# Optimization experiments

Hardware: AMD Instinct MI355X
Metric: run time of the kernel (lower is better)

The kernel has to match this reference:

```python
import jax, jax.numpy as jnp
import numpy as np

B, NQ, C = 2, 10000, 256
M, L, K = 8, 3, 4
D = C // M
LEVEL_SHAPES = [(100, 100), (50, 50), (25, 25)]


def setup_inputs() -> dict:
    key = jax.random.key(0)
    ks = jax.random.split(key, 16)
    inp = {
        "query": jax.random.normal(ks[0], (B, NQ, C), jnp.float32),
        "reference_points": jax.random.uniform(ks[1], (B, NQ, 2), jnp.float32),
        "value0": jax.random.normal(ks[2], (B, C) + LEVEL_SHAPES[0], jnp.float32),
        "value1": jax.random.normal(ks[3], (B, C) + LEVEL_SHAPES[1], jnp.float32),
        "value2": jax.random.normal(ks[4], (B, C) + LEVEL_SHAPES[2], jnp.float32),
        "Wv": jax.random.normal(ks[5], (C, C), jnp.float32) * 0.02,
        "bv": jnp.zeros((C,), jnp.float32),
        "Ws": jax.random.normal(ks[6], (M * L * K * 2, C), jnp.float32) * 0.05,
        "bs": jax.random.normal(ks[7], (M * L * K * 2,), jnp.float32),
        "Wa": jax.random.normal(ks[8], (M * L * K, C), jnp.float32) * 0.02,
        "ba": jnp.zeros((M * L * K,), jnp.float32),
        "Wo": jax.random.normal(ks[9], (C, C), jnp.float32) * 0.02,
        "bo": jnp.zeros((C,), jnp.float32),
    }
    return inp


def _bilinear_sample(vflat, px, py, H, W):
    """grid_sample bilinear, align_corners=False, padding_mode='zeros'.
    vflat: (B, M, H*W, D); px, py: (B, M, Q, K) pixel coords. -> (B, M, Q, K, D)
    """
    b, m, q, k = px.shape
    x0 = jnp.floor(px)
    y0 = jnp.floor(py)
    wx1 = px - x0  # frac weights (grad 1 w.r.t. px, matching grid_sample)
    wy1 = py - y0
    wx0 = 1.0 - wx1
    wy0 = 1.0 - wy1

    def gather(xi, yi):
        valid = ((xi >= 0) & (xi <= W - 1) & (yi >= 0) & (yi <= H - 1)).astype(vflat.dtype)
        xc = jnp.clip(xi, 0, W - 1).astype(jnp.int32)
        yc = jnp.clip(yi, 0, H - 1).astype(jnp.int32)
        idx = (yc * W + xc).reshape(b, m, q * k)
        g = jnp.take_along_axis(vflat, idx[..., None], axis=2)  # (B,M,QK,D)
        return g.reshape(b, m, q, k, -1) * valid[..., None]

    out = (gather(x0, y0) * (wx0 * wy0)[..., None]
           + gather(x0 + 1, y0) * (wx1 * wy0)[..., None]
           + gather(x0, y0 + 1) * (wx0 * wy1)[..., None]
           + gather(x0 + 1, y0 + 1) * (wx1 * wy1)[..., None])
    return out


def reference(query, reference_points, value0, value1, value2,
              Wv, bv, Ws, bs, Wa, ba, Wo, bo):
    bsz, nq, c = query.shape
    dt = query.dtype
    # sampling offsets and attention weights
    off = (query @ Ws.T + bs).reshape(bsz, nq, M, L, K, 2)
    attn = jax.nn.softmax((query @ Wa.T + ba).reshape(bsz, nq, M, L * K), axis=-1)
    attn = attn.reshape(bsz, nq, M, L, K)

    out = jnp.zeros((bsz, nq, M, D), dt)
    for li, v in enumerate([value0, value1, value2]):
        H, W = v.shape[2], v.shape[3]
        # conv1x1 value projection -> per-head maps (B, M, H*W, D)
        proj = jnp.einsum('bchw,oc->bohw', v, Wv) + bv[None, :, None, None]
        vflat = proj.reshape(bsz, M, D, H * W).transpose(0, 1, 3, 2)
        norm = jnp.asarray([W, H], dt)
        loc = reference_points[:, :, None, None, :] + off[:, :, :, li, :, :] / norm  # (B,Q,M,K,2)
        # grid = loc*2-1; pixel = (grid+1)*size/2 - 0.5 = loc*size - 0.5
        px = (loc[..., 0] * W - 0.5).transpose(0, 2, 1, 3)  # (B,M,Q,K)
        py = (loc[..., 1] * H - 0.5).transpose(0, 2, 1, 3)
        sampled = _bilinear_sample(vflat, px, py, H, W)  # (B,M,Q,K,D)
        out = out + jnp.einsum('bmqkd,bqmk->bqmd', sampled, attn[:, :, :, li, :])

    out = out.reshape(bsz, nq, c)
    return out @ Wo.T + bo
```

## Files before the change

kernel.cpp:

```cpp
#include <hip/hip_runtime.h>
#include <cstddef>

#define B_ 2
#define NQ_ 10000
#define C_ 256
#define M_ 8
#define L_ 3
#define K_ 4
#define D_ 32
#define P_ 13125

typedef unsigned short u16;
typedef __attribute__((ext_vector_type(8))) short short8;
typedef __attribute__((ext_vector_type(4))) float f32x4;

static __device__ __forceinline__ u16 f2bf(float f) {
    union { float f; unsigned u; } x; x.f = f;
    unsigned r = x.u + 0x7fffu + ((x.u >> 16) & 1u);
    return (u16)(r >> 16);
}
static __device__ __forceinline__ short8 cvt8(const float4& a, const float4& b) {
    short8 r;
    r[0] = (short)f2bf(a.x); r[1] = (short)f2bf(a.y);
    r[2] = (short)f2bf(a.z); r[3] = (short)f2bf(a.w);
    r[4] = (short)f2bf(b.x); r[5] = (short)f2bf(b.y);
    r[6] = (short)f2bf(b.z); r[7] = (short)f2bf(b.w);
    return r;
}

__global__ __launch_bounds__(256) void cvt_q(
    const float* __restrict__ src, u16* __restrict__ dst)
{
    const int i4 = (blockIdx.x * 256 + threadIdx.x) * 4;
    float4 v = *reinterpret_cast<const float4*>(src + i4);
    ushort4 o;
    o.x = f2bf(v.x); o.y = f2bf(v.y); o.z = f2bf(v.z); o.w = f2bf(v.w);
    *reinterpret_cast<ushort4*>(dst + i4) = o;
}

__global__ __launch_bounds__(256) void proj_fused(
    const float* __restrict__ v0, const float* __restrict__ v1,
    const float* __restrict__ v2,
    const float* __restrict__ Wv, const float* __restrict__ bv,
    u16* __restrict__ proj)
{
    __shared__ u16 As[64 * 264];
    __shared__ u16 Bs[64 * 264];

    const int rowTile = blockIdx.x;
    const int b  = rowTile / 207;
    const int tl = rowTile % 207;
    int p0, HW, base;
    const float* V;
    if (tl < 157)      { p0 = tl * 64;         HW = 10000; base = 0;
                         V = v0 + (size_t)b * 256 * 10000; }
    else if (tl < 197) { p0 = (tl - 157) * 64; HW = 2500;  base = 10000;
                         V = v1 + (size_t)b * 256 * 2500; }
    else               { p0 = (tl - 197) * 64; HW = 625;   base = 12500;
                         V = v2 + (size_t)b * 256 * 625; }

    const int t = threadIdx.x;
    const int px  = t & 63;
    const int pxg = min(p0 + px, HW - 1);
    const int ch0 = t >> 6;
    #pragma unroll
    for (int g = 0; g < 8; ++g) {
        float vv[8];
        #pragma unroll
        for (int j = 0; j < 8; ++j)
            vv[j] = V[(size_t)(ch0 + 4 * (8 * g + j)) * HW + pxg];
        #pragma unroll
        for (int j = 0; j < 8; ++j)
            As[px * 264 + ch0 + 4 * (8 * g + j)] = f2bf(vv[j]);
    }
    __syncthreads();

    const int w  = t >> 6;
    const int l  = t & 63;
    const int lr = l & 15;
    const int kb = (l >> 4) * 8;
    const int arow = w * 16 + lr;

    short8 a[8];
    #pragma unroll
    for (int s = 0; s < 8; ++s)
        a[s] = *reinterpret_cast<const short8*>(&As[arow * 264 + kb + s * 32]);

    for (int p = 0; p < 4; ++p) {
        __syncthreads();
        const int o0 = p * 64;
        #pragma unroll
        for (int i = 0; i < 8; ++i) {
            int idx = i * 256 + t;
            int col = idx >> 5;
            int kc  = (idx & 31) * 8;
            const float* Br = Wv + (size_t)(o0 + col) * 256 + kc;
            float4 f0 = *reinterpret_cast<const float4*>(Br);
            float4 f1 = *reinterpret_cast<const float4*>(Br + 4);
            *reinterpret_cast<short8*>(&Bs[col * 264 + kc]) = cvt8(f0, f1);
        }
        __syncthreads();

        f32x4 acc[4] = {};
        #pragma unroll
        for (int s = 0; s < 8; ++s) {
            const int k0 = s * 32;
            short8 b0 = *reinterpret_cast<const short8*>(&Bs[(0 * 16 + lr) * 264 + kb + k0]);
            short8 b1 = *reinterpret_cast<const short8*>(&Bs[(1 * 16 + lr) * 264 + kb + k0]);
            short8 b2 = *reinterpret_cast<const short8*>(&Bs[(2 * 16 + lr) * 264 + kb + k0]);
            short8 b3 = *reinterpret_cast<const short8*>(&Bs[(3 * 16 + lr) * 264 + kb + k0]);
            acc[0] = __builtin_amdgcn_mfma_f32_16x16x32_bf16(a[s], b0, acc[0], 0, 0, 0);
            acc[1] = __builtin_amdgcn_mfma_f32_16x16x32_bf16(a[s], b1, acc[1], 0, 0, 0);
            acc[2] = __builtin_amdgcn_mfma_f32_16x16x32_bf16(a[s], b2, acc[2], 0, 0, 0);
            acc[3] = __builtin_amdgcn_mfma_f32_16x16x32_bf16(a[s], b3, acc[3], 0, 0, 0);
        }

        const int orow = (l >> 4) * 4;
        #pragma unroll
        for (int ct = 0; ct < 4; ++ct) {
            const int col = o0 + ct * 16 + lr;
            const float bsv = bv[col];
            #pragma unroll
            for (int r = 0; r < 4; ++r) {
                const int prow = w * 16 + orow + r;
                if (p0 + prow < HW)
                    proj[((size_t)b * P_ + base + p0 + prow) * 256 + col] =
                        f2bf(acc[ct][r] + bsv);
            }
        }
    }
}

template <typename OutT>
__global__ __launch_bounds__(256) void gemm_reg(
    const u16* __restrict__ A, int rows, int npanel,
    const float* __restrict__ B1f, const float* __restrict__ bias1, int N1,
    const float* __restrict__ B2f, const float* __restrict__ bias2, int Ntot,
    OutT* __restrict__ Cout)
{
    __shared__ u16 Bs[64 * 264];

    const int rowTile = blockIdx.x / npanel;
    const int panel   = blockIdx.x % npanel;
    const int t  = threadIdx.x;
    const int w  = t >> 6;
    const int l  = t & 63;
    const int lr = l & 15;
    const int kb = (l >> 4) * 8;
    const int o0 = panel * 64;
    const int rbase = rowTile * 256 + w * 64;

    short8 a[4][8];
    #pragma unroll
    for (int f = 0; f < 4; ++f) {
        const int ra = min(rbase + f * 16 + lr, rows - 1);
        const u16* Ap = A + (size_t)ra * 256 + kb;
        #pragma unroll
        for (int s = 0; s < 8; ++s)
            a[f][s] = *reinterpret_cast<const short8*>(Ap + s * 32);
    }

    #pragma unroll
    for (int i = 0; i < 8; ++i) {
        int idx = i * 256 + t;
        int col = idx >> 5;
        int kc  = (idx & 31) * 8;
        int colg = min(o0 + col, Ntot - 1);
        const float* Br = ((colg < N1) ? B1f + (size_t)colg * 256
                                       : B2f + (size_t)(colg - N1) * 256) + kc;
        float4 f0 = *reinterpret_cast<const float4*>(Br);
        float4 f1 = *reinterpret_cast<const float4*>(Br + 4);
        *reinterpret_cast<short8*>(&Bs[col * 264 + kc]) = cvt8(f0, f1);
    }
    __syncthreads();

    f32x4 acc[4][4] = {};

    #pragma unroll
    for (int s = 0; s < 8; ++s) {
        const int k0 = s * 32;
        short8 b0 = *reinterpret_cast<const short8*>(&Bs[(0 * 16 + lr) * 264 + kb + k0]);
        short8 b1 = *reinterpret_cast<const short8*>(&Bs[(1 * 16 + lr) * 264 + kb + k0]);
        short8 b2 = *reinterpret_cast<const short8*>(&Bs[(2 * 16 + lr) * 264 + kb + k0]);
        short8 b3 = *reinterpret_cast<const short8*>(&Bs[(3 * 16 + lr) * 264 + kb + k0]);
        #pragma unroll
        for (int f = 0; f < 4; ++f) {
            acc[f][0] = __builtin_amdgcn_mfma_f32_16x16x32_bf16(a[f][s], b0, acc[f][0], 0, 0, 0);
            acc[f][1] = __builtin_amdgcn_mfma_f32_16x16x32_bf16(a[f][s], b1, acc[f][1], 0, 0, 0);
            acc[f][2] = __builtin_amdgcn_mfma_f32_16x16x32_bf16(a[f][s], b2, acc[f][2], 0, 0, 0);
            acc[f][3] = __builtin_amdgcn_mfma_f32_16x16x32_bf16(a[f][s], b3, acc[f][3], 0, 0, 0);
        }
    }

    const int orow = (l >> 4) * 4;
    #pragma unroll
    for (int ct = 0; ct < 4; ++ct) {
        const int col = o0 + ct * 16 + lr;
        if (col >= Ntot) continue;
        const float bsv = (col < N1) ? bias1[col] : bias2[col - N1];
        #pragma unroll
        for (int f = 0; f < 4; ++f) {
            #pragma unroll
            for (int r = 0; r < 4; ++r) {
                const int row = rbase + f * 16 + orow + r;
                if (row < rows) {
                    float val = acc[f][ct][r] + bsv;
                    if constexpr (sizeof(OutT) == 2)
                        Cout[(size_t)row * Ntot + col] = (OutT)f2bf(val);
                    else
                        Cout[(size_t)row * Ntot + col] = (OutT)val;
                }
            }
        }
    }
}

__global__ __launch_bounds__(256) void sample_kernel(
    const float* __restrict__ S,
    const float* __restrict__ refp,
    const u16* __restrict__ proj,
    u16* __restrict__ out2)
{
    constexpr int Wd[3]   = {100, 50, 25};
    constexpr int offs[3] = {0, 10000, 12500};

    __shared__ int   midx[192][4];
    __shared__ float mw[192][4];

    const int t = threadIdx.x;

    if (t < 192) {
        const int q  = t / 96;
        const int tq = t % 96;
        const int tm = tq / 12;
        const int tj = tq % 12;
        const int bq = blockIdx.x * 2 + q;
        const float* Sq = S + (size_t)bq * 288;

        float lg[12], mx = -1e30f;
        #pragma unroll
        for (int jj = 0; jj < 12; ++jj) {
            lg[jj] = Sq[192 + tm * 12 + jj];
            mx = fmaxf(mx, lg[jj]);
        }
        float sum = 0.f;
        #pragma unroll
        for (int jj = 0; jj < 12; ++jj) sum += __expf(lg[jj] - mx);
        const float attn = __expf(lg[tj] - mx) / sum;

        const int l  = tj >> 2;
        const int Wl = Wd[l];
        const float refx = refp[(size_t)bq * 2 + 0];
        const float refy = refp[(size_t)bq * 2 + 1];
        const float ox = Sq[(tm * 12 + tj) * 2 + 0];
        const float oy = Sq[(tm * 12 + tj) * 2 + 1];
        const float px = refx * (float)Wl + ox - 0.5f;
        const float py = refy * (float)Wl + oy - 0.5f;
        const float x0f = floorf(px), y0f = floorf(py);
        const float wx1 = px - x0f, wy1 = py - y0f;
        const float wx0 = 1.f - wx1, wy0 = 1.f - wy1;
        const int x0 = (int)x0f, y0 = (int)y0f;
        const int x1 = x0 + 1, y1 = y0 + 1;
        const bool vx0 = (unsigned)x0 < (unsigned)Wl;
        const bool vx1 = (unsigned)x1 < (unsigned)Wl;
        const bool vy0 = (unsigned)y0 < (unsigned)Wl;
        const bool vy1 = (unsigned)y1 < (unsigned)Wl;
        const int chb  = tm * 32;
        const int base = offs[l];
        midx[t][0] = (vx0 && vy0) ? ((base + y0 * Wl + x0) * 256 + chb) : 0;
        midx[t][1] = (vx1 && vy0) ? ((base + y0 * Wl + x1) * 256 + chb) : 0;
        midx[t][2] = (vx0 && vy1) ? ((base + y1 * Wl + x0) * 256 + chb) : 0;
        midx[t][3] = (vx1 && vy1) ? ((base + y1 * Wl + x1) * 256 + chb) : 0;
        mw[t][0] = (vx0 && vy0) ? attn * wx0 * wy0 : 0.f;
        mw[t][1] = (vx1 && vy0) ? attn * wx1 * wy0 : 0.f;
        mw[t][2] = (vx0 && vy1) ? attn * wx0 * wy1 : 0.f;
        mw[t][3] = (vx1 && vy1) ? attn * wx1 * wy1 : 0.f;
    }
    __syncthreads();

    const int qi  = t >> 7;
    const int tt  = t & 127;
    const int mh  = tt >> 4;
    const int d16 = tt & 15;
    const int bq2 = blockIdx.x * 2 + qi;
    const int b   = bq2 / NQ_;
    const u16* projb = proj + (size_t)b * P_ * 256 + 2 * d16;

    float acc0 = 0.f, acc1 = 0.f;

    #pragma unroll
    for (int j = 0; j < 12; ++j) {
        const int mj = qi * 96 + mh * 12 + j;
        const int4   o  = *reinterpret_cast<const int4*>(midx[mj]);
        const float4 ww = *reinterpret_cast<const float4*>(mw[mj]);
        const unsigned u00 = *reinterpret_cast<const unsigned*>(projb + o.x);
        const unsigned u10 = *reinterpret_cast<const unsigned*>(projb + o.y);
        const unsigned u01 = *reinterpret_cast<const unsigned*>(projb + o.z);
        const unsigned u11 = *reinterpret_cast<const unsigned*>(projb + o.w);
        union { unsigned u; float f; } c0, c1;
        c0.u = u00 << 16;          c1.u = u00 & 0xffff0000u;
        acc0 = fmaf(ww.x, c0.f, acc0); acc1 = fmaf(ww.x, c1.f, acc1);
        c0.u = u10 << 16;          c1.u = u10 & 0xffff0000u;
        acc0 = fmaf(ww.y, c0.f, acc0); acc1 = fmaf(ww.y, c1.f, acc1);
        c0.u = u01 << 16;          c1.u = u01 & 0xffff0000u;
        acc0 = fmaf(ww.z, c0.f, acc0); acc1 = fmaf(ww.z, c1.f, acc1);
        c0.u = u11 << 16;          c1.u = u11 & 0xffff0000u;
        acc0 = fmaf(ww.w, c0.f, acc0); acc1 = fmaf(ww.w, c1.f, acc1);
    }

    const unsigned packed = (unsigned)f2bf(acc0) | ((unsigned)f2bf(acc1) << 16);
    *reinterpret_cast<unsigned*>(out2 + (size_t)bq2 * 256 + mh * 32 + 2 * d16) = packed;
}

extern "C" void kernel_launch(void* const* d_in, const int* in_sizes, int n_in,
                              void* d_out, int out_size, void* d_ws, size_t ws_size,
                              hipStream_t stream)
{
    const float* query = (const float*)d_in[0];
    const float* refp  = (const float*)d_in[1];
    const float* v0    = (const float*)d_in[2];
    const float* v1    = (const float*)d_in[3];
    const float* v2    = (const float*)d_in[4];
    const float* Wv    = (const float*)d_in[5];
    const float* bv    = (const float*)d_in[6];
    const float* Ws    = (const float*)d_in[7];
    const float* bs    = (const float*)d_in[8];
    const float* Wa    = (const float*)d_in[9];
    const float* ba    = (const float*)d_in[10];
    const float* Wo    = (const float*)d_in[11];
    const float* bo    = (const float*)d_in[12];
    float* out = (float*)d_out;

    char* wsb = (char*)d_ws;
    u16*   proj = (u16*)wsb;    wsb += (size_t)B_ * P_ * 256 * 2;
    float* S    = (float*)wsb;  wsb += (size_t)B_ * NQ_ * 288 * 4;
    u16*   out2 = (u16*)wsb;    wsb += (size_t)B_ * NQ_ * 256 * 2;
    u16*   qbf  = (u16*)wsb;    wsb += (size_t)B_ * NQ_ * 256 * 2;

    dim3 blk(256);

    cvt_q<<<dim3(5000), blk, 0, stream>>>(query, qbf);

    proj_fused<<<dim3(414), blk, 0, stream>>>(v0, v1, v2, Wv, bv, proj);

    gemm_reg<float><<<dim3(79 * 5), blk, 0, stream>>>(
        qbf, B_ * NQ_, 5, Ws, bs, 192, Wa, ba, 288, S);

    sample_kernel<<<dim3(NQ_), blk, 0, stream>>>(S, refp, proj, out2);

    gemm_reg<float><<<dim3(79 * 4), blk, 0, stream>>>(
        out2, B_ * NQ_, 4, Wo, bo, 256, Wo, bo, 256, out);
}
```

Baseline: 206.1 us.

## Fuse query bf16 conversion into offset GEMM and merge with value projection launch

Removes the separate query fp32-to-bf16 conversion kernel by converting query rows in registers inside the offset/attention GEMM. That GEMM and the value projection now run as one launch, with block index selecting the role. This saves two kernel launches and a 10 MB bf16 round trip through memory, and lets both independent GEMMs fill the GPU at the same time. The cost is reading fp32 query directly (twice the bytes per A load) and a heavier kernel with a shared, role-dependent register footprint.

```diff
diff --git a/kernel.cpp b/kernel.cpp
--- a/kernel.cpp
+++ b/kernel.cpp
@@ -28,115 +28,178 @@
     return r;
 }
 
-__global__ __launch_bounds__(256) void cvt_q(
-    const float* __restrict__ src, u16* __restrict__ dst)
-{
-    const int i4 = (blockIdx.x * 256 + threadIdx.x) * 4;
-    float4 v = *reinterpret_cast<const float4*>(src + i4);
-    ushort4 o;
-    o.x = f2bf(v.x); o.y = f2bf(v.y); o.z = f2bf(v.z); o.w = f2bf(v.w);
-    *reinterpret_cast<ushort4*>(dst + i4) = o;
-}
-
-__global__ __launch_bounds__(256) void proj_fused(
+__global__ __launch_bounds__(256) void phase_a(
     const float* __restrict__ v0, const float* __restrict__ v1,
     const float* __restrict__ v2,
     const float* __restrict__ Wv, const float* __restrict__ bv,
-    u16* __restrict__ proj)
+    const float* __restrict__ query,
+    const float* __restrict__ Ws, const float* __restrict__ bs,
+    const float* __restrict__ Wa, const float* __restrict__ ba,
+    u16* __restrict__ proj, float* __restrict__ S)
 {
     __shared__ u16 As[64 * 264];
     __shared__ u16 Bs[64 * 264];
 
-    const int rowTile = blockIdx.x;
-    const int b  = rowTile / 207;
-    const int tl = rowTile % 207;
-    int p0, HW, base;
-    const float* V;
-    if (tl < 157)      { p0 = tl * 64;         HW = 10000; base = 0;
-                         V = v0 + (size_t)b * 256 * 10000; }
-    else if (tl < 197) { p0 = (tl - 157) * 64; HW = 2500;  base = 10000;
-                         V = v1 + (size_t)b * 256 * 2500; }
-    else               { p0 = (tl - 197) * 64; HW = 625;   base = 12500;
-                         V = v2 + (size_t)b * 256 * 625; }
-
-    const int t = threadIdx.x;
-    const int px  = t & 63;
-    const int pxg = min(p0 + px, HW - 1);
-    const int ch0 = t >> 6;
-    #pragma unroll
-    for (int g = 0; g < 8; ++g) {
-        float vv[8];
-        #pragma unroll
-        for (int j = 0; j < 8; ++j)
-            vv[j] = V[(size_t)(ch0 + 4 * (8 * g + j)) * HW + pxg];
-        #pragma unroll
-        for (int j = 0; j < 8; ++j)
-            As[px * 264 + ch0 + 4 * (8 * g + j)] = f2bf(vv[j]);
-    }
-    __syncthreads();
-
+    const int t  = threadIdx.x;
     const int w  = t >> 6;
     const int l  = t & 63;
     const int lr = l & 15;
     const int kb = (l >> 4) * 8;
-    const int arow = w * 16 + lr;
-
-    short8 a[8];
-    #pragma unroll
-    for (int s = 0; s < 8; ++s)
-        a[s] = *reinterpret_cast<const short8*>(&As[arow * 264 + kb + s * 32]);
-
-    for (int p = 0; p < 4; ++p) {
+
+    if (blockIdx.x < 414) {
+        const int rowTile = blockIdx.x;
+        const int b  = rowTile / 207;
+        const int tl = rowTile % 207;
+        int p0, HW, base;
+        const float* V;
+        if (tl < 157)      { p0 = tl * 64;         HW = 10000; base = 0;
+                             V = v0 + (size_t)b * 256 * 10000; }
+        else if (tl < 197) { p0 = (tl - 157) * 64; HW = 2500;  base = 10000;
+                             V = v1 + (size_t)b * 256 * 2500; }
+        else               { p0 = (tl - 197) * 64; HW = 625;   base = 12500;
+                             V = v2 + (size_t)b * 256 * 625; }
+
+        const int px  = t & 63;
+        const int pxg = min(p0 + px, HW - 1);
+        const int ch0 = t >> 6;
+        #pragma unroll
+        for (int g = 0; g < 8; ++g) {
+            float vv[8];
+            #pragma unroll
+            for (int j = 0; j < 8; ++j)
+                vv[j] = V[(size_t)(ch0 + 4 * (8 * g + j)) * HW + pxg];
+            #pragma unroll
+            for (int j = 0; j < 8; ++j)
+                As[px * 264 + ch0 + 4 * (8 * g + j)] = f2bf(vv[j]);
+        }
         __syncthreads();
-        const int o0 = p * 64;
-        #pragma unroll
-        for (int i = 0; i < 8; ++i) {
-            int idx = i * 256 + t;
-            int col = idx >> 5;
-            int kc  = (idx & 31) * 8;
-            const float* Br = Wv + (size_t)(o0 + col) * 256 + kc;
-            float4 f0 = *reinterpret_cast<const float4*>(Br);
-            float4 f1 = *reinterpret_cast<const float4*>(Br + 4);
-            *reinterpret_cast<short8*>(&Bs[col * 264 + kc]) = cvt8(f0, f1);
-        }
-        __syncthreads();
-
-        f32x4 acc[4] = {};
+
+        const int arow = w * 16 + lr;
+        short8 a[8];
+        #pragma unroll
+        for (int s = 0; s < 8; ++s)
+            a[s] = *reinterpret_cast<const short8*>(&As[arow * 264 + kb + s * 32]);
+
+        for (int p = 0; p < 4; ++p) {
+            __syncthreads();
+            const int o0 = p * 64;
+            #pragma unroll
+            for (int i = 0; i < 8; ++i) {
+                int idx = i * 256 + t;
+                int col = idx >> 5;
+                int kc  = (idx & 31) * 8;
+                const float* Br = Wv + (size_t)(o0 + col) * 256 + kc;
+                float4 f0 = *reinterpret_cast<const float4*>(Br);
+                float4 f1 = *reinterpret_cast<const float4*>(Br + 4);
+                *reinterpret_cast<short8*>(&Bs[col * 264 + kc]) = cvt8(f0, f1);
+            }
+            __syncthreads();
+
+            f32x4 acc[4] = {};
+            #pragma unroll
+            for (int s = 0; s < 8; ++s) {
+                const int k0 = s * 32;
+                short8 b0 = *reinterpret_cast<const short8*>(&Bs[(0 * 16 + lr) * 264 + kb + k0]);
+                short8 b1 = *reinterpret_cast<const short8*>(&Bs[(1 * 16 + lr) * 264 + kb + k0]);
+                short8 b2 = *reinterpret_cast<const short8*>(&Bs[(2 * 16 + lr) * 264 + kb + k0]);
+                short8 b3 = *reinterpret_cast<const short8*>(&Bs[(3 * 16 + lr) * 264 + kb + k0]);
+                acc[0] = __builtin_amdgcn_mfma_f32_16x16x32_bf16(a[s], b0, acc[0], 0, 0, 0);
+                acc[1] = __builtin_amdgcn_mfma_f32_16x16x32_bf16(a[s], b1, acc[1], 0, 0, 0);
+                acc[2] = __builtin_amdgcn_mfma_f32_16x16x32_bf16(a[s], b2, acc[2], 0, 0, 0);
+                acc[3] = __builtin_amdgcn_mfma_f32_16x16x32_bf16(a[s], b3, acc[3], 0, 0, 0);
+            }
+
+            const int orow = (l >> 4) * 4;
+            #pragma unroll
+            for (int ct = 0; ct < 4; ++ct) {
+                const int col = o0 + ct * 16 + lr;
+                const float bsv = bv[col];
+                #pragma unroll
+                for (int r = 0; r < 4; ++r) {
+                    const int prow = w * 16 + orow + r;
+                    if (p0 + prow < HW)
+                        proj[((size_t)b * P_ + base + p0 + prow) * 256 + col] =
+                            f2bf(acc[ct][r] + bsv);
+                }
+            }
+        }
+        return;
+    }
+
+    const int g = blockIdx.x - 414;
+    const int rowTile = g / 5;
+    const int panel   = g % 5;
+    const int o0    = panel * 64;
+    const int rbase = rowTile * 256 + w * 64;
+    const int rows  = B_ * NQ_;
+    constexpr int N1 = 192, Ntot = 288;
+
+    short8 a[4][8];
+    #pragma unroll
+    for (int f = 0; f < 4; ++f) {
+        const int ra = min(rbase + f * 16 + lr, rows - 1);
+        const float* Ap = query + (size_t)ra * 256 + kb;
         #pragma unroll
         for (int s = 0; s < 8; ++s) {
-            const int k0 = s * 32;
-            short8 b0 = *reinterpret_cast<const short8*>(&Bs[(0 * 16 + lr) * 264 + kb + k0]);
-            short8 b1 = *reinterpret_cast<const short8*>(&Bs[(1 * 16 + lr) * 264 + kb + k0]);
-            short8 b2 = *reinterpret_cast<const short8*>(&Bs[(2 * 16 + lr) * 264 + kb + k0]);
-            short8 b3 = *reinterpret_cast<const short8*>(&Bs[(3 * 16 + lr) * 264 + kb + k0]);
-            acc[0] = __builtin_amdgcn_mfma_f32_16x16x32_bf16(a[s], b0, acc[0], 0, 0, 0);
-            acc[1] = __builtin_amdgcn_mfma_f32_16x16x32_bf16(a[s], b1, acc[1], 0, 0, 0);
-            acc[2] = __builtin_amdgcn_mfma_f32_16x16x32_bf16(a[s], b2, acc[2], 0, 0, 0);
-            acc[3] = __builtin_amdgcn_mfma_f32_16x16x32_bf16(a[s], b3, acc[3], 0, 0, 0);
-        }
-
-        const int orow = (l >> 4) * 4;
-        #pragma unroll
-        for (int ct = 0; ct < 4; ++ct) {
-            const int col = o0 + ct * 16 + lr;
-            const float bsv = bv[col];
+            float4 x = *reinterpret_cast<const float4*>(Ap + s * 32);
+            float4 y = *reinterpret_cast<const float4*>(Ap + s * 32 + 4);
+            a[f][s] = cvt8(x, y);
+        }
+    }
+
+    #pragma unroll
+    for (int i = 0; i < 8; ++i) {
+        int idx = i * 256 + t;
+        int col = idx >> 5;
+        int kc  = (idx & 31) * 8;
+        int colg = min(o0 + col, Ntot - 1);
+        const float* Br = ((colg < N1) ? Ws + (size_t)colg * 256
+                                       : Wa + (size_t)(colg - N1) * 256) + kc;
+        float4 f0 = *reinterpret_cast<const float4*>(Br);
+        float4 f1 = *reinterpret_cast<const float4*>(Br + 4);
+        *reinterpret_cast<short8*>(&Bs[col * 264 + kc]) = cvt8(f0, f1);
+    }
+    __syncthreads();
+
+    f32x4 acc[4][4] = {};
+    #pragma unroll
+    for (int s = 0; s < 8; ++s) {
+        const int k0 = s * 32;
+        short8 b0 = *reinterpret_cast<const short8*>(&Bs[(0 * 16 + lr) * 264 + kb + k0]);
+        short8 b1 = *reinterpret_cast<const short8*>(&Bs[(1 * 16 + lr) * 264 + kb + k0]);
+        short8 b2 = *reinterpret_cast<const short8*>(&Bs[(2 * 16 + lr) * 264 + kb + k0]);
+        short8 b3 = *reinterpret_cast<const short8*>(&Bs[(3 * 16 + lr) * 264 + kb + k0]);
+        #pragma unroll
+        for (int f = 0; f < 4; ++f) {
+            acc[f][0] = __builtin_amdgcn_mfma_f32_16x16x32_bf16(a[f][s], b0, acc[f][0], 0, 0, 0);
+            acc[f][1] = __builtin_amdgcn_mfma_f32_16x16x32_bf16(a[f][s], b1, acc[f][1], 0, 0, 0);
+            acc[f][2] = __builtin_amdgcn_mfma_f32_16x16x32_bf16(a[f][s], b2, acc[f][2], 0, 0, 0);
+            acc[f][3] = __builtin_amdgcn_mfma_f32_16x16x32_bf16(a[f][s], b3, acc[f][3], 0, 0, 0);
+        }
+    }
+
+    const int orow = (l >> 4) * 4;
+    #pragma unroll
+    for (int ct = 0; ct < 4; ++ct) {
+        const int col = o0 + ct * 16 + lr;
+        if (col >= Ntot) continue;
+        const float bsv = (col < N1) ? bs[col] : ba[col - N1];
+        #pragma unroll
+        for (int f = 0; f < 4; ++f) {
             #pragma unroll
             for (int r = 0; r < 4; ++r) {
-                const int prow = w * 16 + orow + r;
-                if (p0 + prow < HW)
-                    proj[((size_t)b * P_ + base + p0 + prow) * 256 + col] =
-                        f2bf(acc[ct][r] + bsv);
+                const int row = rbase + f * 16 + orow + r;
+                if (row < rows)
+                    S[(size_t)row * Ntot + col] = acc[f][ct][r] + bsv;
             }
         }
     }
 }
 
-template <typename OutT>
 __global__ __launch_bounds__(256) void gemm_reg(
     const u16* __restrict__ A, int rows, int npanel,
-    const float* __restrict__ B1f, const float* __restrict__ bias1, int N1,
-    const float* __restrict__ B2f, const float* __restrict__ bias2, int Ntot,
-    OutT* __restrict__ Cout)
+    const float* __restrict__ Bf, const float* __restrict__ bias, int Ntot,
+    float* __restrict__ Cout)
 {
     __shared__ u16 Bs[64 * 264];
 
@@ -165,9 +228,7 @@
         int idx = i * 256 + t;
         int col = idx >> 5;
         int kc  = (idx & 31) * 8;
-        int colg = min(o0 + col, Ntot - 1);
-        const float* Br = ((colg < N1) ? B1f + (size_t)colg * 256
-                                       : B2f + (size_t)(colg - N1) * 256) + kc;
+        const float* Br = Bf + (size_t)(o0 + col) * 256 + kc;
         float4 f0 = *reinterpret_cast<const float4*>(Br);
         float4 f1 = *reinterpret_cast<const float4*>(Br + 4);
         *reinterpret_cast<short8*>(&Bs[col * 264 + kc]) = cvt8(f0, f1);
@@ -175,7 +236,6 @@
     __syncthreads();
 
     f32x4 acc[4][4] = {};
-
     #pragma unroll
     for (int s = 0; s < 8; ++s) {
         const int k0 = s * 32;
@@ -196,20 +256,14 @@
     #pragma unroll
     for (int ct = 0; ct < 4; ++ct) {
         const int col = o0 + ct * 16 + lr;
-        if (col >= Ntot) continue;
-        const float bsv = (col < N1) ? bias1[col] : bias2[col - N1];
+        const float bsv = bias[col];
         #pragma unroll
         for (int f = 0; f < 4; ++f) {
             #pragma unroll
             for (int r = 0; r < 4; ++r) {
                 const int row = rbase + f * 16 + orow + r;
-                if (row < rows) {
-                    float val = acc[f][ct][r] + bsv;
-                    if constexpr (sizeof(OutT) == 2)
-                        Cout[(size_t)row * Ntot + col] = (OutT)f2bf(val);
-                    else
-                        Cout[(size_t)row * Ntot + col] = (OutT)val;
-                }
+                if (row < rows)
+                    Cout[(size_t)row * Ntot + col] = acc[f][ct][r] + bsv;
             }
         }
     }
@@ -335,19 +389,14 @@
     u16*   proj = (u16*)wsb;    wsb += (size_t)B_ * P_ * 256 * 2;
     float* S    = (float*)wsb;  wsb += (size_t)B_ * NQ_ * 288 * 4;
     u16*   out2 = (u16*)wsb;    wsb += (size_t)B_ * NQ_ * 256 * 2;
-    u16*   qbf  = (u16*)wsb;    wsb += (size_t)B_ * NQ_ * 256 * 2;
 
     dim3 blk(256);
 
-    cvt_q<<<dim3(5000), blk, 0, stream>>>(query, qbf);
-
-    proj_fused<<<dim3(414), blk, 0, stream>>>(v0, v1, v2, Wv, bv, proj);
-
-    gemm_reg<float><<<dim3(79 * 5), blk, 0, stream>>>(
-        qbf, B_ * NQ_, 5, Ws, bs, 192, Wa, ba, 288, S);
+    phase_a<<<dim3(809), blk, 0, stream>>>(v0, v1, v2, Wv, bv,
+                                           query, Ws, bs, Wa, ba, proj, S);
 
     sample_kernel<<<dim3(NQ_), blk, 0, stream>>>(S, refp, proj, out2);
 
-    gemm_reg<float><<<dim3(79 * 4), blk, 0, stream>>>(
-        out2, B_ * NQ_, 4, Wo, bo, 256, Wo, bo, 256, out);
-}
+    gemm_reg<<<dim3(79 * 4), blk, 0, stream>>>(
+        out2, B_ * NQ_, 4, Wo, bo, 256, out);
+}
```

Result: slower. 225.3 us (+9.3%).
